# Kernel optimization log

Hardware: AMD Instinct MI355X
Metric: run time of the kernel (lower is better)

The kernel has to match this reference:

```python
import jax, jax.numpy as jnp
import numpy as np

N, OUT, IN = 16384, 2048, 2048

def setup_inputs() -> dict:
    key = jax.random.key(0)
    k1, k2, k3 = jax.random.split(key, 3)
    input_ = jax.random.normal(k1, (N, IN), dtype=jnp.float32)
    # kaiming normal, fan_in mode: std = sqrt(2/fan_in)
    weight = jax.random.normal(k2, (OUT, IN), dtype=jnp.float32) * np.sqrt(2.0 / IN)
    mask = jax.random.randint(k3, (OUT, IN), 0, 2, dtype=jnp.int32)
    return {"input_": input_, "weight": weight, "mask": mask}

def reference(input_, weight, mask):
    # out = x @ (W * mask)^T  -- mask is a fixed binary expander pattern
    masked_w = weight * mask.astype(weight.dtype)  # [OUT, IN]
    return jnp.matmul(input_, masked_w.T)          # [N, OUT]
```

## Files before the change

### kernel.cpp

```cpp
#include <hip/hip_runtime.h>


#define MDIM 16384
#define NDIM 2048
#define KDIM 2048

#define BM 256
#define BN 256
#define NITER (KDIM / 128)
#define GRID_X ((MDIM / BM) * (NDIM / BN))

using f32x4   = __attribute__((ext_vector_type(4))) float;
using bf16x8  = __attribute__((ext_vector_type(8))) __bf16;
using ushort8 = __attribute__((ext_vector_type(8))) unsigned short;

__device__ __forceinline__ unsigned short f2bf(float f) {
  unsigned int u = __builtin_bit_cast(unsigned int, f);
  u = u + 0x7FFFu + ((u >> 16) & 1u);
  return (unsigned short)(u >> 16);
}


__global__ void convert_input_kernel(const float* __restrict__ in,
                                     unsigned short* __restrict__ out) {
  size_t base = ((size_t)blockIdx.x * blockDim.x + threadIdx.x) * 8;
  float4 a = *reinterpret_cast<const float4*>(in + base);
  float4 b = *reinterpret_cast<const float4*>(in + base + 4);
  ushort8 v;
  v[0] = f2bf(a.x); v[1] = f2bf(a.y); v[2] = f2bf(a.z); v[3] = f2bf(a.w);
  v[4] = f2bf(b.x); v[5] = f2bf(b.y); v[6] = f2bf(b.z); v[7] = f2bf(b.w);
  *reinterpret_cast<ushort8*>(out + base) = v;
}

__global__ void convert_weight_kernel(const float* __restrict__ w,
                                      const int* __restrict__ mk,
                                      unsigned short* __restrict__ out) {
  size_t base = ((size_t)blockIdx.x * blockDim.x + threadIdx.x) * 8;
  float4 a = *reinterpret_cast<const float4*>(w + base);
  float4 b = *reinterpret_cast<const float4*>(w + base + 4);
  int4 m0 = *reinterpret_cast<const int4*>(mk + base);
  int4 m1 = *reinterpret_cast<const int4*>(mk + base + 4);
  ushort8 v;
  v[0] = m0.x ? f2bf(a.x) : (unsigned short)0;
  v[1] = m0.y ? f2bf(a.y) : (unsigned short)0;
  v[2] = m0.z ? f2bf(a.z) : (unsigned short)0;
  v[3] = m0.w ? f2bf(a.w) : (unsigned short)0;
  v[4] = m1.x ? f2bf(b.x) : (unsigned short)0;
  v[5] = m1.y ? f2bf(b.y) : (unsigned short)0;
  v[6] = m1.z ? f2bf(b.z) : (unsigned short)0;
  v[7] = m1.w ? f2bf(b.w) : (unsigned short)0;
  *reinterpret_cast<ushort8*>(out + base) = v;
}


__device__ __forceinline__ f32x4 MF(bf16x8 a, bf16x8 b, f32x4 c) {
  return __builtin_amdgcn_mfma_f32_16x16x32_bf16(a, b, c, 0, 0, 0);
}
__device__ __forceinline__ void bar() {
  asm volatile("" ::: "memory");
  __builtin_amdgcn_s_barrier();
  asm volatile("" ::: "memory");
}
#define VMCNT(n) asm volatile("s_waitcnt vmcnt(" #n ")" ::: "memory")

__global__ __launch_bounds__(512, 2) void gemm8p(
    const unsigned short* __restrict__ Abf,
    const unsigned short* __restrict__ Bbf,
    float* __restrict__ C) {
  __shared__ __attribute__((aligned(16))) unsigned short Asl[4 * 8192];
  __shared__ __attribute__((aligned(16))) unsigned short Bsl[4 * 8192];

  int bid = blockIdx.x;
  int wgs = (bid & 7) * (GRID_X / 8) + (bid >> 3);
  int tm = wgs >> 3;
  int tn = wgs & 7;
  int row0 = tm * BM, col0 = tn * BN;

  int t = threadIdx.x;
  int lane = t & 63, wid = t >> 6;
  int wr = wid >> 2, wc = wid & 3;
  int fr = lane & 15, fq = lane >> 4;

  int p0 = (wid * 2 + 0) * 64 + lane;
  int p1 = (wid * 2 + 1) * 64 + lane;
  int r0 = p0 >> 2, kc0 = ((p0 & 3) ^ ((r0 >> 1) & 3)) * 8;
  int r1 = p1 >> 2, kc1 = ((p1 & 3) ^ ((r1 >> 1) & 3)) * 8;
  size_t offA0 = (size_t)(row0 + r0) * KDIM + kc0;
  size_t offA1 = (size_t)(row0 + r1) * KDIM + kc1;
  size_t offB0 = (size_t)(col0 + r0) * KDIM + kc0;
  size_t offB1 = (size_t)(col0 + r1) * KDIM + kc1;
  int ldsw0 = (wid * 2 + 0) * 512;
  int ldsw1 = (wid * 2 + 1) * 512;

  int kxor = (fq ^ ((fr >> 1) & 3)) * 8;
  int aoff = (wr * 128 + fr) * 32 + kxor;
  int boff = (wc * 64 + fr) * 32 + kxor;

  f32x4 acc[8][4];
#pragma unroll
  for (int m = 0; m < 8; ++m)
#pragma unroll
    for (int n = 0; n < 4; ++n) acc[m][n] = f32x4{0.f, 0.f, 0.f, 0.f};
  bf16x8 afr[8];

#define SLOT_A(b, kh) (Asl + ((b) * 2 + (kh)) * 8192)
#define SLOT_B(b, kh) (Bsl + ((b) * 2 + (kh)) * 8192)

#define STG(slot, base, o0, o1, ke) do {                                        \
  __builtin_amdgcn_global_load_lds(                                             \
      (const __attribute__((address_space(1))) void*)((base) + (o0) + (ke)),    \
      (__attribute__((address_space(3))) void*)((slot) + ldsw0), 16, 0, 0);     \
  __builtin_amdgcn_global_load_lds(                                             \
      (const __attribute__((address_space(1))) void*)((base) + (o1) + (ke)),    \
      (__attribute__((address_space(3))) void*)((slot) + ldsw1), 16, 0, 0);     \
} while (0)

#define PHASE(b, kh, nh, STAGES, WAITS) do {                                    \
  if ((nh) == 0) {                                                              \
    const unsigned short* _ap = SLOT_A(b, kh) + aoff;                           \
    _Pragma("unroll")                                                           \
    for (int _m = 0; _m < 8; ++_m) afr[_m] = *(const bf16x8*)(_ap + _m * 512);  \
  }                                                                             \
  const unsigned short* _bp = SLOT_B(b, kh) + boff + (nh) * 1024;               \
  bf16x8 _b0 = *(const bf16x8*)(_bp);                                           \
  bf16x8 _b1 = *(const bf16x8*)(_bp + 512);                                     \
  STAGES;                                                                       \
  WAITS;                                                                        \
  bar();                                                                        \
  __builtin_amdgcn_s_setprio(1);                                                \
  _Pragma("unroll")                                                             \
  for (int _m = 0; _m < 8; ++_m) {                                              \
    acc[_m][(nh) * 2]     = MF(afr[_m], _b0, acc[_m][(nh) * 2]);                \
    acc[_m][(nh) * 2 + 1] = MF(afr[_m], _b1, acc[_m][(nh) * 2 + 1]);            \
  }                                                                             \
  __builtin_amdgcn_s_setprio(0);                                                \
  bar();                                                                        \
} while (0)

  STG(SLOT_A(0, 0), Abf, offA0, offA1, 0);
  STG(SLOT_B(0, 0), Bbf, offB0, offB1, 0);
  STG(SLOT_A(0, 1), Abf, offA0, offA1, 32);
  STG(SLOT_B(0, 1), Bbf, offB0, offB1, 32);
  STG(SLOT_A(1, 0), Abf, offA0, offA1, 64);
  STG(SLOT_B(1, 0), Bbf, offB0, offB1, 64);
  VMCNT(4);
  bar();

  for (int i = 0; i < NITER - 1; ++i) {
    int kb = i * 128;
    PHASE(0, 0, 0, { STG(SLOT_A(1, 1), Abf, offA0, offA1, kb + 96);
                     STG(SLOT_B(1, 1), Bbf, offB0, offB1, kb + 96); }, );
    PHASE(0, 0, 1, , );
    PHASE(0, 1, 0, STG(SLOT_A(0, 0), Abf, offA0, offA1, kb + 128), );
    PHASE(0, 1, 1, STG(SLOT_B(0, 0), Bbf, offB0, offB1, kb + 128), VMCNT(4));
    PHASE(1, 0, 0, { STG(SLOT_A(0, 1), Abf, offA0, offA1, kb + 160);
                     STG(SLOT_B(0, 1), Bbf, offB0, offB1, kb + 160); }, );
    PHASE(1, 0, 1, , );
    PHASE(1, 1, 0, STG(SLOT_A(1, 0), Abf, offA0, offA1, kb + 192), );
    PHASE(1, 1, 1, STG(SLOT_B(1, 0), Bbf, offB0, offB1, kb + 192), VMCNT(4));
  }
  {
    int kb = (NITER - 1) * 128;
    PHASE(0, 0, 0, { STG(SLOT_A(1, 1), Abf, offA0, offA1, kb + 96);
                     STG(SLOT_B(1, 1), Bbf, offB0, offB1, kb + 96); }, );
    PHASE(0, 0, 1, , );
    PHASE(0, 1, 0, , );
    PHASE(0, 1, 1, , VMCNT(0));
    PHASE(1, 0, 0, , );
    PHASE(1, 0, 1, , );
    PHASE(1, 1, 0, , );
    PHASE(1, 1, 1, , );
  }

  size_t crow = (size_t)(row0 + wr * 128 + fq * 4);
  int ccol = col0 + wc * 64 + fr;
#pragma unroll
  for (int m = 0; m < 8; ++m)
#pragma unroll
    for (int n = 0; n < 4; ++n) {
      float* cp = C + (crow + m * 16) * NDIM + ccol + n * 16;
#pragma unroll
      for (int e = 0; e < 4; ++e) cp[(size_t)e * NDIM] = acc[m][n][e];
    }
#undef PHASE
#undef STG
#undef SLOT_A
#undef SLOT_B
}


__global__ __launch_bounds__(256) void gemm_fused_fallback(
    const float* __restrict__ Afp,
    const float* __restrict__ Wfp,
    const int* __restrict__ Mk,
    float* __restrict__ C) {
  __shared__ unsigned short As[128 * 32];
  __shared__ unsigned short Bs[128 * 32];
  int bid = blockIdx.x;
  int nwg = (MDIM / 128) * (NDIM / 128);
  int wg = (bid & 7) * (nwg / 8) + (bid >> 3);
  int tm = wg >> 4, tn = wg & 15;
  int row0 = tm * 128, col0 = tn * 128;
  int t = threadIdx.x;
  int lane = t & 63, wv = t >> 6;
  int wr = wv >> 1, wc = wv & 1;
  int fr = lane & 15, fq = lane >> 4;
  f32x4 acc[4][4];
#pragma unroll
  for (int i = 0; i < 4; ++i)
#pragma unroll
    for (int j = 0; j < 4; ++j) acc[i][j] = f32x4{0.f, 0.f, 0.f, 0.f};
  for (int kt = 0; kt < KDIM; kt += 32) {
#pragma unroll
    for (int j = 0; j < 2; ++j) {
      int c = j * 256 + t;
      int r = c >> 2;
      int ko = (c & 3) * 8;
      const float* ga = Afp + (size_t)(row0 + r) * KDIM + kt + ko;
      float4 a0 = *reinterpret_cast<const float4*>(ga);
      float4 a1 = *reinterpret_cast<const float4*>(ga + 4);
      ushort8 va;
      va[0] = f2bf(a0.x); va[1] = f2bf(a0.y); va[2] = f2bf(a0.z); va[3] = f2bf(a0.w);
      va[4] = f2bf(a1.x); va[5] = f2bf(a1.y); va[6] = f2bf(a1.z); va[7] = f2bf(a1.w);
      *reinterpret_cast<ushort8*>(As + (size_t)c * 8) = va;
      const float* gw = Wfp + (size_t)(col0 + r) * KDIM + kt + ko;
      const int* gm = Mk + (size_t)(col0 + r) * KDIM + kt + ko;
      float4 w0 = *reinterpret_cast<const float4*>(gw);
      float4 w1 = *reinterpret_cast<const float4*>(gw + 4);
      int4 m0 = *reinterpret_cast<const int4*>(gm);
      int4 m1 = *reinterpret_cast<const int4*>(gm + 4);
      ushort8 vb;
      vb[0] = m0.x ? f2bf(w0.x) : (unsigned short)0;
      vb[1] = m0.y ? f2bf(w0.y) : (unsigned short)0;
      vb[2] = m0.z ? f2bf(w0.z) : (unsigned short)0;
      vb[3] = m0.w ? f2bf(w0.w) : (unsigned short)0;
      vb[4] = m1.x ? f2bf(w1.x) : (unsigned short)0;
      vb[5] = m1.y ? f2bf(w1.y) : (unsigned short)0;
      vb[6] = m1.z ? f2bf(w1.z) : (unsigned short)0;
      vb[7] = m1.w ? f2bf(w1.w) : (unsigned short)0;
      *reinterpret_cast<ushort8*>(Bs + (size_t)c * 8) = vb;
    }
    __syncthreads();
    bf16x8 af[4], bfr[4];
#pragma unroll
    for (int m2 = 0; m2 < 4; ++m2)
      af[m2] = *reinterpret_cast<const bf16x8*>(As + (wr * 64 + m2 * 16 + fr) * 32 + fq * 8);
#pragma unroll
    for (int n2 = 0; n2 < 4; ++n2)
      bfr[n2] = *reinterpret_cast<const bf16x8*>(Bs + (wc * 64 + n2 * 16 + fr) * 32 + fq * 8);
#pragma unroll
    for (int m2 = 0; m2 < 4; ++m2)
#pragma unroll
      for (int n2 = 0; n2 < 4; ++n2)
        acc[m2][n2] = MF(af[m2], bfr[n2], acc[m2][n2]);
    __syncthreads();
  }
#pragma unroll
  for (int m2 = 0; m2 < 4; ++m2)
#pragma unroll
    for (int n2 = 0; n2 < 4; ++n2) {
      size_t r0 = (size_t)(row0 + wr * 64 + m2 * 16 + fq * 4);
      size_t c0 = (size_t)(col0 + wc * 64 + n2 * 16 + fr);
#pragma unroll
      for (int i = 0; i < 4; ++i) C[(r0 + i) * NDIM + c0] = acc[m2][n2][i];
    }
}


extern "C" void kernel_launch(void* const* d_in, const int* in_sizes, int n_in,
                              void* d_out, int out_size, void* d_ws, size_t ws_size,
                              hipStream_t stream) {
  const float* input  = (const float*)d_in[0];
  const float* weight = (const float*)d_in[1];
  const int*   mask   = (const int*)d_in[2];
  float* out = (float*)d_out;

  const size_t needA = (size_t)MDIM * KDIM * sizeof(unsigned short);
  const size_t needB = (size_t)NDIM * KDIM * sizeof(unsigned short);

  if (ws_size >= needA + needB) {
    unsigned short* Abf = (unsigned short*)d_ws;
    unsigned short* Bbf = (unsigned short*)((char*)d_ws + needA);
    convert_input_kernel<<<(MDIM * (size_t)KDIM / 8) / 256, 256, 0, stream>>>(input, Abf);
    convert_weight_kernel<<<(NDIM * (size_t)KDIM / 8) / 256, 256, 0, stream>>>(weight, mask, Bbf);
    gemm8p<<<GRID_X, 512, 0, stream>>>(Abf, Bbf, out);
  } else {
    int nwg = (MDIM / 128) * (NDIM / 128);
    gemm_fused_fallback<<<nwg, 256, 0, stream>>>(input, weight, mask, out);
  }
}
```

Before: 180.4 us.

## Merge GEMM main loop from eight half-phases into four full K-slot phases

Each phase now loads all eight A fragments and four B fragments for one K-slot and issues the full 8x4 MFMA block, where before each slot was split into two N-halves. This halves the number of barrier pairs per K iteration. Global-to-LDS staging is reshuffled so each phase issues both the A and B loads for a future slot, with vmcnt waits adjusted to match. The cost is higher register pressure from holding twelve fragments at once, and less overlap granularity between loads and MFMAs.

```diff
diff --git a/kernel.cpp b/kernel.cpp
--- a/kernel.cpp
+++ b/kernel.cpp
@@ -63,7 +63,7 @@
 }
 #define VMCNT(n) asm volatile("s_waitcnt vmcnt(" #n ")" ::: "memory")
 
-__global__ __launch_bounds__(512, 2) void gemm8p(
+__global__ __launch_bounds__(512, 2) void gemm4p(
     const unsigned short* __restrict__ Abf,
     const unsigned short* __restrict__ Bbf,
     float* __restrict__ C) {
@@ -101,7 +101,6 @@
   for (int m = 0; m < 8; ++m)
 #pragma unroll
     for (int n = 0; n < 4; ++n) acc[m][n] = f32x4{0.f, 0.f, 0.f, 0.f};
-  bf16x8 afr[8];
 
 #define SLOT_A(b, kh) (Asl + ((b) * 2 + (kh)) * 8192)
 #define SLOT_B(b, kh) (Bsl + ((b) * 2 + (kh)) * 8192)
@@ -115,24 +114,24 @@
       (__attribute__((address_space(3))) void*)((slot) + ldsw1), 16, 0, 0);     \
 } while (0)
 
-#define PHASE(b, kh, nh, STAGES, WAITS) do {                                    \
-  if ((nh) == 0) {                                                              \
-    const unsigned short* _ap = SLOT_A(b, kh) + aoff;                           \
-    _Pragma("unroll")                                                           \
-    for (int _m = 0; _m < 8; ++_m) afr[_m] = *(const bf16x8*)(_ap + _m * 512);  \
-  }                                                                             \
-  const unsigned short* _bp = SLOT_B(b, kh) + boff + (nh) * 1024;               \
-  bf16x8 _b0 = *(const bf16x8*)(_bp);                                           \
-  bf16x8 _b1 = *(const bf16x8*)(_bp + 512);                                     \
+#define PHASE(b, kh, STAGES, WAITS) do {                                        \
+  const unsigned short* _ap = SLOT_A(b, kh) + aoff;                             \
+  const unsigned short* _bp = SLOT_B(b, kh) + boff;                             \
+  bf16x8 _afr[8], _bfr[4];                                                      \
+  _afr[0] = *(const bf16x8*)(_ap);                                              \
+  _Pragma("unroll")                                                             \
+  for (int _n = 0; _n < 4; ++_n) _bfr[_n] = *(const bf16x8*)(_bp + _n * 512);   \
+  _Pragma("unroll")                                                             \
+  for (int _m = 1; _m < 8; ++_m) _afr[_m] = *(const bf16x8*)(_ap + _m * 512);   \
   STAGES;                                                                       \
   WAITS;                                                                        \
   bar();                                                                        \
   __builtin_amdgcn_s_setprio(1);                                                \
   _Pragma("unroll")                                                             \
-  for (int _m = 0; _m < 8; ++_m) {                                              \
-    acc[_m][(nh) * 2]     = MF(afr[_m], _b0, acc[_m][(nh) * 2]);                \
-    acc[_m][(nh) * 2 + 1] = MF(afr[_m], _b1, acc[_m][(nh) * 2 + 1]);            \
-  }                                                                             \
+  for (int _m = 0; _m < 8; ++_m)                                                \
+    _Pragma("unroll")                                                           \
+    for (int _n = 0; _n < 4; ++_n)                                              \
+      acc[_m][_n] = MF(_afr[_m], _bfr[_n], acc[_m][_n]);                        \
   __builtin_amdgcn_s_setprio(0);                                                \
   bar();                                                                        \
 } while (0)
@@ -143,33 +142,27 @@
   STG(SLOT_B(0, 1), Bbf, offB0, offB1, 32);
   STG(SLOT_A(1, 0), Abf, offA0, offA1, 64);
   STG(SLOT_B(1, 0), Bbf, offB0, offB1, 64);
-  VMCNT(4);
+  VMCNT(8);
   bar();
 
   for (int i = 0; i < NITER - 1; ++i) {
     int kb = i * 128;
-    PHASE(0, 0, 0, { STG(SLOT_A(1, 1), Abf, offA0, offA1, kb + 96);
-                     STG(SLOT_B(1, 1), Bbf, offB0, offB1, kb + 96); }, );
-    PHASE(0, 0, 1, , );
-    PHASE(0, 1, 0, STG(SLOT_A(0, 0), Abf, offA0, offA1, kb + 128), );
-    PHASE(0, 1, 1, STG(SLOT_B(0, 0), Bbf, offB0, offB1, kb + 128), VMCNT(4));
-    PHASE(1, 0, 0, { STG(SLOT_A(0, 1), Abf, offA0, offA1, kb + 160);
-                     STG(SLOT_B(0, 1), Bbf, offB0, offB1, kb + 160); }, );
-    PHASE(1, 0, 1, , );
-    PHASE(1, 1, 0, STG(SLOT_A(1, 0), Abf, offA0, offA1, kb + 192), );
-    PHASE(1, 1, 1, STG(SLOT_B(1, 0), Bbf, offB0, offB1, kb + 192), VMCNT(4));
+    PHASE(0, 0, { STG(SLOT_A(1, 1), Abf, offA0, offA1, kb + 96);
+                  STG(SLOT_B(1, 1), Bbf, offB0, offB1, kb + 96); }, VMCNT(8));
+    PHASE(0, 1, { STG(SLOT_A(0, 0), Abf, offA0, offA1, kb + 128);
+                  STG(SLOT_B(0, 0), Bbf, offB0, offB1, kb + 128); }, VMCNT(8));
+    PHASE(1, 0, { STG(SLOT_A(0, 1), Abf, offA0, offA1, kb + 160);
+                  STG(SLOT_B(0, 1), Bbf, offB0, offB1, kb + 160); }, VMCNT(8));
+    PHASE(1, 1, { STG(SLOT_A(1, 0), Abf, offA0, offA1, kb + 192);
+                  STG(SLOT_B(1, 0), Bbf, offB0, offB1, kb + 192); }, VMCNT(8));
   }
   {
     int kb = (NITER - 1) * 128;
-    PHASE(0, 0, 0, { STG(SLOT_A(1, 1), Abf, offA0, offA1, kb + 96);
-                     STG(SLOT_B(1, 1), Bbf, offB0, offB1, kb + 96); }, );
-    PHASE(0, 0, 1, , );
-    PHASE(0, 1, 0, , );
-    PHASE(0, 1, 1, , VMCNT(0));
-    PHASE(1, 0, 0, , );
-    PHASE(1, 0, 1, , );
-    PHASE(1, 1, 0, , );
-    PHASE(1, 1, 1, , );
+    PHASE(0, 0, { STG(SLOT_A(1, 1), Abf, offA0, offA1, kb + 96);
+                  STG(SLOT_B(1, 1), Bbf, offB0, offB1, kb + 96); }, VMCNT(8));
+    PHASE(0, 1, , VMCNT(4));
+    PHASE(1, 0, , VMCNT(0));
+    PHASE(1, 1, , );
   }
 
   size_t crow = (size_t)(row0 + wr * 128 + fq * 4);
@@ -283,7 +276,7 @@
     unsigned short* Bbf = (unsigned short*)((char*)d_ws + needA);
     convert_input_kernel<<<(MDIM * (size_t)KDIM / 8) / 256, 256, 0, stream>>>(input, Abf);
     convert_weight_kernel<<<(NDIM * (size_t)KDIM / 8) / 256, 256, 0, stream>>>(weight, mask, Bbf);
-    gemm8p<<<GRID_X, 512, 0, stream>>>(Abf, Bbf, out);
+    gemm4p<<<GRID_X, 512, 0, stream>>>(Abf, Bbf, out);
   } else {
     int nwg = (MDIM / 128) * (NDIM / 128);
     gemm_fused_fallback<<<nwg, 256, 0, stream>>>(input, weight, mask, out);
```

New measurement: 182.4 us. Within noise of the previous version (+1.1%).
